# Kernel optimization log

Hardware: AMD Instinct MI355X
Metric: run time of the kernel (lower is better)

The kernel has to match this reference:

```python
import jax, jax.numpy as jnp
import numpy as np

V, D, HID, HOPS = 50000, 300, 300, 2
H = HID // 2  # per-direction hidden (bi_direction=True)
B, NT, SL, HL = 32, 20, 50, 50


def _gen_data():
    rng = np.random.default_rng(0)
    tc = np.zeros((B, NT, 3 + SL), np.int32)
    for b in range(B):
        tn = int(rng.integers(5, NT + 1))
        for t in range(tn):
            tc[b, t, :3] = rng.integers(1, 10, 3)
            sl = int(rng.integers(5, SL + 1))
            tc[b, t, 3:3 + sl] = rng.integers(1, V, sl)
    uh = np.zeros((B, HL, SL), np.int32)
    for b in range(B):
        hn = int(rng.integers(10, HL + 1))
        for s in range(hn):
            sl = int(rng.integers(5, SL + 1))
            uh[b, s, :sl] = rng.integers(1, V, sl)
    return jnp.asarray(tc), jnp.asarray(uh)


def setup_inputs():
    key = jax.random.key(0)
    ks = jax.random.split(key, 12)
    tc, uh = _gen_data()
    E = jax.random.normal(ks[0], (V, D), jnp.float32) * 0.05
    E = E.at[0].set(0.0)  # padding_idx=0
    nA = HOPS + 1  # hop_num+1 SentLSTM encoders (A[0] is also B)
    return {
        "target_conv": tc, "user_history": uh, "E": E,
        "A_Wih": jax.random.normal(ks[1], (nA, 2, 4 * H, D), jnp.float32) * 0.05,
        "A_Whh": jax.random.normal(ks[2], (nA, 2, 4 * H, H), jnp.float32) * 0.05,
        "A_bih": jax.random.normal(ks[3], (nA, 2, 4 * H), jnp.float32) * 0.05,
        "A_bhh": jax.random.normal(ks[4], (nA, 2, 4 * H), jnp.float32) * 0.05,
        "C_Wih": jax.random.normal(ks[5], (2, 4 * H, HID + 3), jnp.float32) * 0.05,
        "C_Whh": jax.random.normal(ks[6], (2, 4 * H, H), jnp.float32) * 0.05,
        "C_bih": jax.random.normal(ks[7], (2, 4 * H), jnp.float32) * 0.05,
        "C_bhh": jax.random.normal(ks[8], (2, 4 * H), jnp.float32) * 0.05,
        "W_out": jax.random.normal(ks[9], (HID,), jnp.float32) * 0.05,
        "b_out": jnp.zeros((), jnp.float32),
    }


def _lstm_final(x, lens, Wih, Whh, bih, bhh):
    """Masked-length LSTM over padded batch. x:[N,T,Din] -> final h:[N,H].
    PyTorch gate order i,f,g,o. Zero initial state. Updates frozen at t>=len."""
    N, T, _ = x.shape
    gx = jnp.einsum('ntd,gd->ntg', x, Wih) + bih  # input projection once

    def step(carry, inp):
        h, c = carry
        g_t, t = inp
        g = g_t + h @ Whh.T + bhh
        i, f, gg, o = jnp.split(g, 4, axis=-1)
        c_new = jax.nn.sigmoid(f) * c + jax.nn.sigmoid(i) * jnp.tanh(gg)
        h_new = jax.nn.sigmoid(o) * jnp.tanh(c_new)
        m = (t < lens)[:, None]
        return (jnp.where(m, h_new, h), jnp.where(m, c_new, c)), None

    h0 = jnp.zeros((N, Whh.shape[1]), x.dtype)
    (h, _), _ = jax.lax.scan(step, (h0, h0), (gx.transpose(1, 0, 2), jnp.arange(T)))
    return h


def _bilstm_final(x, lens, Wih, Whh, bih, bhh):
    """Bidirectional final hidden = concat(h_fwd_last_valid, h_bwd_after_full_reverse).
    Equivalent to pack_padded_sequence + nn.LSTM(bidirectional=True) final hidden."""
    T = x.shape[1]
    hf = _lstm_final(x, lens, Wih[0], Whh[0], bih[0], bhh[0])
    idx = jnp.clip(lens[:, None] - 1 - jnp.arange(T)[None, :], 0, T - 1)  # per-sample reverse
    hb = _lstm_final(jnp.take_along_axis(x, idx[:, :, None], axis=1), lens,
                     Wih[1], Whh[1], bih[1], bhh[1])
    return jnp.concatenate([hf, hb], axis=-1)


def reference(target_conv, user_history, E, A_Wih, A_Whh, A_bih, A_bhh,
              C_Wih, C_Whh, C_bih, C_bhh, W_out, b_out):
    # --- encode target conversation turns with B = A[0] ---
    tok = target_conv[:, :, 3:]                      # [B,NT,SL]
    slens = jnp.sum(tok != 0, -1).reshape(-1)        # ragged sentence lengths
    x = E[tok.reshape(B * NT, SL)]                   # [B*NT,SL,D]
    sent_reps = _bilstm_final(x, slens, A_Wih[0], A_Whh[0], A_bih[0], A_bhh[0]).reshape(B, NT, HID)
    feats = jnp.concatenate([sent_reps, target_conv[:, :, :3].astype(jnp.float32)], -1)  # [B,NT,HID+3]
    clens = jnp.sum(target_conv[:, :, 3] != 0, -1)   # valid turns per conv
    u = _bilstm_final(feats, clens, C_Wih, C_Whh, C_bih, C_bhh)  # [B,HID]
    # --- memory hops over user history ---
    hlens = jnp.sum(user_history != 0, -1).reshape(-1)
    hx = E[user_history.reshape(B * HL, SL)]
    reps = [_bilstm_final(hx, hlens, A_Wih[k], A_Whh[k], A_bih[k], A_bhh[k]).reshape(B, HL, HID)
            for k in range(HOPS + 1)]                # invalid sents have len=0 -> zero reps (matches zero-padding)
    for hop in range(HOPS):
        prob = jax.nn.softmax(jnp.einsum('bnd,bd->bn', reps[hop], u), -1)
        u = jnp.einsum('bn,bnd->bd', prob, reps[hop + 1]) + u
    return jax.nn.sigmoid(u @ W_out + b_out)
```

## Files before the change

### kernel.cpp

```cpp
#include <hip/hip_runtime.h>
#include <hip/hip_cooperative_groups.h>

typedef short v8s __attribute__((ext_vector_type(8)));
typedef float v4f __attribute__((ext_vector_type(4)));
typedef unsigned short ushort_t;
typedef unsigned int uint_t;

namespace cg = cooperative_groups;

__device__ inline ushort_t f2bf(float f) {
    union { float f; uint_t u; } v; v.f = f;
    uint_t r = v.u + 0x7FFFu + ((v.u >> 16) & 1u);
    return (ushort_t)(r >> 16);
}
__device__ inline float bf2f(ushort_t h) {
    union { uint_t u; float f; } v; v.u = ((uint_t)h) << 16;
    return v.f;
}
__device__ inline float sigf(float x) { return 1.f / (1.f + __expf(-x)); }
__device__ inline float tanh_f(float x) {
    float e = __expf(-2.f * x);
    return (1.f - e) / (1.f + e);
}

__global__ void k_lens(const int* __restrict__ tc, const int* __restrict__ uh,
                       int* lens_s, int* lens_h, int* lens_c) {
    int t = blockIdx.x * 256 + threadIdx.x;
    if (t < 640) {
        int c = 0;
        for (int s = 0; s < 50; ++s) c += (tc[t * 53 + 3 + s] != 0);
        lens_s[t] = c;
    } else if (t < 2240) {
        int r = t - 640; int c = 0;
        for (int s = 0; s < 50; ++s) c += (uh[r * 50 + s] != 0);
        lens_h[r] = c;
    } else if (t < 2272) {
        int b = t - 2240; int c = 0;
        for (int tt = 0; tt < 20; ++tt) c += (tc[(b * 20 + tt) * 53 + 3] != 0);
        lens_c[b] = c;
    }
}

__global__ void k_sort(const int* __restrict__ lens, int n,
                       int* __restrict__ perm, int* __restrict__ slen) {
    int i = blockIdx.x * 256 + threadIdx.x;
    if (i >= n) return;
    int li = lens[i]; int r = 0;
    for (int j = 0; j < n; ++j) {
        int lj = lens[j];
        r += (lj > li) || (lj == li && j < i);
    }
    perm[r] = i; slen[r] = li;
}

__global__ void k_packA(const float* __restrict__ Wih, const float* __restrict__ Whh,
                        const float* __restrict__ bih, const float* __restrict__ bhh,
                        ushort_t* __restrict__ pack) {
    int job = blockIdx.x; int lane = threadIdx.x;
    int set = job / 570; int rem = job % 570; int tile = rem / 15; int kc = rem % 15;
    int np = tile * 16 + (lane & 15);
    int g = np & 3, d = np >> 2;
    int orig = g * 150 + d;
    int kbase = kc * 32 + (lane >> 4) * 8;
    ushort_t v[8];
#pragma unroll
    for (int j = 0; j < 8; ++j) {
        int k = kbase + j; float f = 0.f;
        if (np < 600) {
            if (k < 300) f = Wih[((size_t)set * 600 + orig) * 300 + k];
            else if (k == 300) f = bih[set * 600 + orig] + bhh[set * 600 + orig];
            else if (k >= 320 && k < 470) f = Whh[((size_t)set * 600 + orig) * 150 + (k - 320)];
        }
        v[j] = f2bf(f);
    }
    uint4 u;
    u.x = (uint_t)v[0] | ((uint_t)v[1] << 16);
    u.y = (uint_t)v[2] | ((uint_t)v[3] << 16);
    u.z = (uint_t)v[4] | ((uint_t)v[5] << 16);
    u.w = (uint_t)v[6] | ((uint_t)v[7] << 16);
    *(uint4*)(pack + ((size_t)job * 64 + lane) * 8) = u;
}

__global__ void k_packC(const float* __restrict__ Wih, const float* __restrict__ Whh,
                        const float* __restrict__ bih, const float* __restrict__ bhh,
                        ushort_t* __restrict__ pack) {
    int job = blockIdx.x; int lane = threadIdx.x;
    int dir = job / 570; int rem = job % 570; int tile = rem / 15; int kc = rem % 15;
    int np = tile * 16 + (lane & 15);
    int g = np & 3, d = np >> 2;
    int orig = g * 150 + d;
    int kbase = kc * 32 + (lane >> 4) * 8;
    ushort_t v[8];
#pragma unroll
    for (int j = 0; j < 8; ++j) {
        int k = kbase + j; float f = 0.f;
        if (np < 600) {
            if (k < 303) f = Wih[((size_t)dir * 600 + orig) * 303 + k];
            else if (k == 303) f = bih[dir * 600 + orig] + bhh[dir * 600 + orig];
            else if (k >= 320 && k < 470) f = Whh[((size_t)dir * 600 + orig) * 150 + (k - 320)];
        }
        v[j] = f2bf(f);
    }
    uint4 u;
    u.x = (uint_t)v[0] | ((uint_t)v[1] << 16);
    u.y = (uint_t)v[2] | ((uint_t)v[3] << 16);
    u.z = (uint_t)v[4] | ((uint_t)v[5] << 16);
    u.w = (uint_t)v[6] | ((uint_t)v[7] << 16);
    *(uint4*)(pack + ((size_t)job * 64 + lane) * 8) = u;
}

__launch_bounds__(512, 2)
__global__ void k_main(const int* __restrict__ tcg, const int* __restrict__ uhg,
                       const float* __restrict__ E,
                       const int* __restrict__ perm_s, const int* __restrict__ slen_s,
                       const int* __restrict__ perm_h, const int* __restrict__ hlen_s,
                       const ushort_t* __restrict__ packA,
                       ushort_t* __restrict__ gx,
                       float* __restrict__ srep, float* __restrict__ reps,
                       int TC, int nchunks) {
    const int bid = blockIdx.x;
    const int tid = threadIdx.x;
    const int lane = tid & 63, w = tid >> 6, q = lane >> 4, l16 = lane & 15;

    __shared__ ushort_t H[64][168];
    __shared__ __align__(16) float Gp[8][16][68];

    const int isrec = (bid < 170);
    int r_pos0 = 0, r_windex = 0, r_dir = 0;
    const int* r_lenv = slen_s; const int* r_permv = perm_s;
    float* r_outp = srep;
    if (isrec) {
        if (bid < 20) {
            int grp = bid / 10; r_dir = grp; r_windex = grp; r_pos0 = (bid % 10) * 64;
            r_lenv = slen_s; r_permv = perm_s; r_outp = srep;
        } else {
            int gh = (bid - 20) / 25; r_windex = gh; r_dir = gh & 1;
            r_pos0 = ((bid - 20) % 25) * 64;
            r_lenv = hlen_s; r_permv = perm_h;
            r_outp = reps + (size_t)(gh >> 1) * 1600 * 300;
        }
        for (int i = tid; i < 64 * 84; i += 512) ((uint_t*)H)[i] = 0u;
    }
    int len4[4];
    if (isrec) {
#pragma unroll
        for (int i = 0; i < 4; ++i) len4[i] = r_lenv[r_pos0 + l16 + 16 * i];
    }
    float cst[5][4];
#pragma unroll
    for (int j = 0; j < 5; ++j)
#pragma unroll
        for (int i = 0; i < 4; ++i) cst[j][i] = 0.f;

    cg::grid_group grid = cg::this_grid();

    for (int c = 0; c < nchunks; ++c) {
        const int tcs0 = 50 - c * TC;
        const int tcs = tcs0 < TC ? tcs0 : TC;
        {
            const int nstepblk = (tcs + 3) / 4;
            const int njobs = 170 * nstepblk;
            for (int job = bid; job < njobs; job += 256) {
                int gj = job % 170; int sb = job / 170;
                const int* lenv; const int* permv; int pos0, windex, dir, isS;
                if (gj < 20) {
                    int grp = gj / 10; dir = grp; windex = grp; pos0 = (gj % 10) * 64;
                    lenv = slen_s; permv = perm_s; isS = 1;
                } else {
                    int gh = (gj - 20) / 25; windex = gh; dir = gh & 1;
                    pos0 = ((gj - 20) % 25) * 64;
                    lenv = hlen_s; permv = perm_h; isS = 0;
                }
                if (lenv[pos0] <= c * TC) continue;
                int lt = sb * 4 + (w >> 1);
                if (lt >= tcs) continue;
                int t = c * TC + lt;
                const int mh = (w & 1) * 2;

                v8s a[2][10];
#pragma unroll
                for (int mg = 0; mg < 2; ++mg) {
                    int pos = pos0 + (mh + mg) * 16 + l16;
                    int len = lenv[pos];
                    int tau = dir ? (len - 1 - t) : t;
                    tau = tau < 0 ? 0 : (tau > 49 ? 49 : tau);
                    int orig = permv[pos];
                    int tok = isS ? tcg[orig * 53 + 3 + tau] : uhg[orig * 50 + tau];
                    const float* Er = E + (size_t)tok * 300;
#pragma unroll
                    for (int kc = 0; kc < 9; ++kc) {
                        int k0 = kc * 32 + q * 8;
                        float4 f0 = *(const float4*)(Er + k0);
                        float4 f1 = *(const float4*)(Er + k0 + 4);
                        v8s r;
                        r[0] = (short)f2bf(f0.x); r[1] = (short)f2bf(f0.y);
                        r[2] = (short)f2bf(f0.z); r[3] = (short)f2bf(f0.w);
                        r[4] = (short)f2bf(f1.x); r[5] = (short)f2bf(f1.y);
                        r[6] = (short)f2bf(f1.z); r[7] = (short)f2bf(f1.w);
                        a[mg][kc] = r;
                    }
                    {
                        v8s r = (v8s){0,0,0,0,0,0,0,0};
                        if (q == 0) {
                            float4 f0 = *(const float4*)(Er + 288);
                            float4 f1 = *(const float4*)(Er + 292);
                            r[0] = (short)f2bf(f0.x); r[1] = (short)f2bf(f0.y);
                            r[2] = (short)f2bf(f0.z); r[3] = (short)f2bf(f0.w);
                            r[4] = (short)f2bf(f1.x); r[5] = (short)f2bf(f1.y);
                            r[6] = (short)f2bf(f1.z); r[7] = (short)f2bf(f1.w);
                        } else if (q == 1) {
                            float4 f0 = *(const float4*)(Er + 296);
                            r[0] = (short)f2bf(f0.x); r[1] = (short)f2bf(f0.y);
                            r[2] = (short)f2bf(f0.z); r[3] = (short)f2bf(f0.w);
                            r[4] = (short)0x3F80;
                        }
                        a[mg][9] = r;
                    }
                }

                const ushort_t* W = packA + (size_t)windex * 570 * 512;
                ushort_t* gout = gx + ((size_t)gj * TC + lt) * 38 * 1024;

                v8s bA[10], bB[10];
                auto loadB = [&](v8s* dst, int tn) {
                    const ushort_t* p = W + (size_t)tn * 15 * 512 + lane * 8;
#pragma unroll
                    for (int kc = 0; kc < 10; ++kc) dst[kc] = *(const v8s*)(p + (size_t)kc * 512);
                };
                auto compute = [&](int tn, v8s* b) {
                    v4f acc[2];
#pragma unroll
                    for (int mg = 0; mg < 2; ++mg) acc[mg] = (v4f){0.f, 0.f, 0.f, 0.f};
#pragma unroll
                    for (int kc = 0; kc < 10; ++kc)
#pragma unroll
                        for (int mg = 0; mg < 2; ++mg)
                            acc[mg] = __builtin_amdgcn_mfma_f32_16x16x32_bf16(a[mg][kc], b[kc], acc[mg], 0, 0, 0);
                    ushort_t* gt = gout + tn * 1024 + l16;
#pragma unroll
                    for (int mg = 0; mg < 2; ++mg)
#pragma unroll
                        for (int r = 0; r < 4; ++r)
                            gt[((mh + mg) * 16 + q * 4 + r) * 16] = f2bf(acc[mg][r]);
                };
                loadB(bA, 0);
                for (int tn = 0; tn < 38; tn += 2) {
                    loadB(bB, tn + 1 < 38 ? tn + 1 : 37);
                    compute(tn, bA);
                    loadB(bA, tn + 2 < 38 ? tn + 2 : 37);
                    compute(tn + 1, bB);
                }
            }
        }
        grid.sync();
        if (isrec) {
            int blockmax = r_lenv[r_pos0];
            int steps = blockmax - c * TC;
            steps = steps < 0 ? 0 : (steps > tcs ? tcs : steps);
            if (steps > 0) {
                const ushort_t* wslot = packA + (size_t)r_windex * 570 * 512;
                const ushort_t* gslot = gx + (size_t)bid * TC * 38 * 1024;
                auto loadW = [&](int j, v8s (&dst)[5]) {
                    int tn = w + 8 * j; int tnc = tn > 37 ? 37 : tn;
                    const ushort_t* wp = wslot + (size_t)tnc * 15 * 512 + lane * 8;
#pragma unroll
                    for (int kc = 0; kc < 5; ++kc) dst[kc] = *(const v8s*)(wp + (size_t)(10 + kc) * 512);
                };
                for (int lt = 0; lt < steps; ++lt) {
                    int t = c * TC + lt;
                    const ushort_t* gstep = gslot + (size_t)lt * 38 * 1024;
                    auto loadG = [&](int j, ushort4 (&dst)[4]) {
                        int tn = w + 8 * j; int tnc = tn > 37 ? 37 : tn;
                        const ushort_t* gb = gstep + (size_t)tnc * 1024 + q * 4;
#pragma unroll
                        for (int i = 0; i < 4; ++i)
                            dst[i] = *(const ushort4*)(gb + (l16 + 16 * i) * 16);
                    };
                    v8s wbA[5], wbB[5];
                    ushort4 gqA[4], gqB[4];
                    loadW(0, wbA); loadG(0, gqA);
                    __syncthreads();
                    v8s ah[4][5];
#pragma unroll
                    for (int mtg = 0; mtg < 4; ++mtg)
#pragma unroll
                        for (int kc = 0; kc < 5; ++kc)
                            ah[mtg][kc] = *(const v8s*)&H[mtg * 16 + l16][kc * 32 + q * 8];
                    __syncthreads();
                    auto jbody = [&](int j, v8s (&wcur)[5], ushort4 (&gcur)[4],
                                     v8s (&wnxt)[5], ushort4 (&gnxt)[4]) {
                        if (j < 4) { loadW(j + 1, wnxt); loadG(j + 1, gnxt); }
                        int tn = w + 8 * j;
                        if (tn < 38) {
                            v4f acc[4];
#pragma unroll
                            for (int mtg = 0; mtg < 4; ++mtg) acc[mtg] = (v4f){0.f, 0.f, 0.f, 0.f};
#pragma unroll
                            for (int kc = 0; kc < 5; ++kc)
#pragma unroll
                                for (int mtg = 0; mtg < 4; ++mtg)
                                    acc[mtg] = __builtin_amdgcn_mfma_f32_16x16x32_bf16(ah[mtg][kc], wcur[kc], acc[mtg], 0, 0, 0);
#pragma unroll
                            for (int mtg = 0; mtg < 4; ++mtg)
                                *(v4f*)&Gp[w][l16][mtg * 16 + q * 4] = acc[mtg];
                            int d = 4 * tn + q;
#pragma unroll
                            for (int i = 0; i < 4; ++i) {
                                int m = l16 + 16 * i;
                                if (t < len4[i]) {
                                    float gi = bf2f(gcur[i].x) + Gp[w][q * 4 + 0][m];
                                    float gf = bf2f(gcur[i].y) + Gp[w][q * 4 + 1][m];
                                    float gg = bf2f(gcur[i].z) + Gp[w][q * 4 + 2][m];
                                    float go = bf2f(gcur[i].w) + Gp[w][q * 4 + 3][m];
                                    float cn = sigf(gf) * cst[j][i] + sigf(gi) * tanh_f(gg);
                                    cst[j][i] = cn;
                                    if (d < 150) H[m][d] = f2bf(sigf(go) * tanh_f(cn));
                                }
                            }
                        }
                    };
                    jbody(0, wbA, gqA, wbB, gqB);
                    jbody(1, wbB, gqB, wbA, gqA);
                    jbody(2, wbA, gqA, wbB, gqB);
                    jbody(3, wbB, gqB, wbA, gqA);
                    jbody(4, wbA, gqA, wbB, gqB);
                }
                __syncthreads();
            }
        }
        grid.sync();
    }
    if (isrec) {
        int m = tid >> 3, dc = tid & 7;
        int orig = r_permv[r_pos0 + m];
#pragma unroll
        for (int k = 0; k < 19; ++k) {
            int d = dc + 8 * k;
            if (d < 150) r_outp[(size_t)orig * 300 + r_dir * 150 + d] = bf2f(H[m][d]);
        }
    }
}

__launch_bounds__(256, 1)
__global__ void k_gxc(const float* __restrict__ srep, const int* __restrict__ tcg,
                      const int* __restrict__ lens_c, const ushort_t* __restrict__ packC,
                      ushort_t* __restrict__ gxc) {
    const int dir = blockIdx.y;
    const int R0 = blockIdx.x * 256;
    const int tnbase = blockIdx.z * 2;
    const int tid = threadIdx.x, lane = tid & 63, w = tid >> 6, q = lane >> 4, l16 = lane & 15;

    v8s a[4][10];
#pragma unroll
    for (int mtg = 0; mtg < 4; ++mtg) {
        int R = R0 + w * 64 + mtg * 16 + l16;
        R = R < 639 ? R : 639;
        int b = R / 20, t = R % 20;
        int clen = lens_c[b];
        int te = dir ? (clen - 1 - t) : t;
        te = te < 0 ? 0 : (te > 19 ? 19 : te);
        const float* sr = srep + (size_t)(b * 20 + te) * 300;
        const int* ft = tcg + (size_t)(b * 20 + te) * 53;
#pragma unroll
        for (int kc = 0; kc < 9; ++kc) {
            int k0 = kc * 32 + q * 8;
            float4 f0 = *(const float4*)(sr + k0);
            float4 f1 = *(const float4*)(sr + k0 + 4);
            v8s r;
            r[0] = (short)f2bf(f0.x); r[1] = (short)f2bf(f0.y);
            r[2] = (short)f2bf(f0.z); r[3] = (short)f2bf(f0.w);
            r[4] = (short)f2bf(f1.x); r[5] = (short)f2bf(f1.y);
            r[6] = (short)f2bf(f1.z); r[7] = (short)f2bf(f1.w);
            a[mtg][kc] = r;
        }
        {
            v8s r = (v8s){0,0,0,0,0,0,0,0};
            if (q == 0) {
                float4 f0 = *(const float4*)(sr + 288);
                float4 f1 = *(const float4*)(sr + 292);
                r[0] = (short)f2bf(f0.x); r[1] = (short)f2bf(f0.y);
                r[2] = (short)f2bf(f0.z); r[3] = (short)f2bf(f0.w);
                r[4] = (short)f2bf(f1.x); r[5] = (short)f2bf(f1.y);
                r[6] = (short)f2bf(f1.z); r[7] = (short)f2bf(f1.w);
            } else if (q == 1) {
                float4 f0 = *(const float4*)(sr + 296);
                r[0] = (short)f2bf(f0.x); r[1] = (short)f2bf(f0.y);
                r[2] = (short)f2bf(f0.z); r[3] = (short)f2bf(f0.w);
                r[4] = (short)f2bf((float)ft[0]);
                r[5] = (short)f2bf((float)ft[1]);
                r[6] = (short)f2bf((float)ft[2]);
                r[7] = (short)0x3F80;
            }
            a[mtg][9] = r;
        }
    }
    const ushort_t* W = packC + (size_t)dir * 570 * 512;
    v8s bA[10];
    auto loadB = [&](v8s* dst, int tn) {
        const ushort_t* p = W + (size_t)tn * 15 * 512 + lane * 8;
#pragma unroll
        for (int kc = 0; kc < 10; ++kc) dst[kc] = *(const v8s*)(p + (size_t)kc * 512);
    };
    auto compute = [&](int tn, v8s* b) {
        v4f acc[4];
#pragma unroll
        for (int mtg = 0; mtg < 4; ++mtg) acc[mtg] = (v4f){0.f, 0.f, 0.f, 0.f};
#pragma unroll
        for (int kc = 0; kc < 10; ++kc)
#pragma unroll
            for (int mtg = 0; mtg < 4; ++mtg)
                acc[mtg] = __builtin_amdgcn_mfma_f32_16x16x32_bf16(a[mtg][kc], b[kc], acc[mtg], 0, 0, 0);
#pragma unroll
        for (int mtg = 0; mtg < 4; ++mtg)
#pragma unroll
            for (int r = 0; r < 4; ++r) {
                int R = R0 + w * 64 + mtg * 16 + q * 4 + r;
                if (R < 640) {
                    int b = R / 20, t = R % 20;
                    gxc[(((size_t)(dir * 20 + t) * 38 + tn) << 9) + b * 16 + l16] = f2bf(acc[mtg][r]);
                }
            }
    };
    for (int tn = tnbase; tn < tnbase + 2; ++tn) {
        loadB(bA, tn);
        compute(tn, bA);
    }
}

__launch_bounds__(256, 1)
__global__ void k_rec_c(const ushort_t* __restrict__ gxc, const int* __restrict__ lens_c,
                        const ushort_t* __restrict__ packC, float* __restrict__ out) {
    const int dir = blockIdx.x;
    const int tid = threadIdx.x, lane = tid & 63, w = tid >> 6, q = lane >> 4, l16 = lane & 15;

    __shared__ ushort_t H[32][168];
    __shared__ __align__(16) float Gp[4][16][68];
    __shared__ int lensl[32];
    __shared__ int mxs;

    if (tid < 32) lensl[tid] = lens_c[tid];
    for (int i = tid; i < 32 * 84; i += 256) ((uint_t*)H)[i] = 0u;
    __syncthreads();
    if (tid == 0) {
        int mx = 0;
        for (int i = 0; i < 32; ++i) mx = max(mx, lensl[i]);
        mxs = mx;
    }
    __syncthreads();
    const int maxlen = mxs;
    int len2[2];
#pragma unroll
    for (int i = 0; i < 2; ++i) len2[i] = lensl[i * 16 + l16];

    v8s wb[10][5];
#pragma unroll
    for (int j = 0; j < 10; ++j) {
        int tn = w + 4 * j; int tnc = tn > 37 ? 37 : tn;
        const ushort_t* wp = packC + (size_t)dir * 570 * 512 + (size_t)tnc * 15 * 512 + lane * 8;
#pragma unroll
        for (int kc = 0; kc < 5; ++kc) wb[j][kc] = *(const v8s*)(wp + (size_t)(10 + kc) * 512);
    }
    float cst[10][2];
#pragma unroll
    for (int j = 0; j < 10; ++j)
#pragma unroll
        for (int i = 0; i < 2; ++i) cst[j][i] = 0.f;

    for (int t = 0; t < maxlen; ++t) {
        __syncthreads();
        v8s ah[2][5];
#pragma unroll
        for (int mtg = 0; mtg < 2; ++mtg)
#pragma unroll
            for (int kc = 0; kc < 5; ++kc)
                ah[mtg][kc] = *(const v8s*)&H[mtg * 16 + l16][kc * 32 + q * 8];
        __syncthreads();
#pragma unroll
        for (int j = 0; j < 10; ++j) {
            int tn = w + 4 * j;
            if (tn < 38) {
                v4f acc[2];
#pragma unroll
                for (int mtg = 0; mtg < 2; ++mtg) acc[mtg] = (v4f){0.f, 0.f, 0.f, 0.f};
#pragma unroll
                for (int kc = 0; kc < 5; ++kc)
#pragma unroll
                    for (int mtg = 0; mtg < 2; ++mtg)
                        acc[mtg] = __builtin_amdgcn_mfma_f32_16x16x32_bf16(ah[mtg][kc], wb[j][kc], acc[mtg], 0, 0, 0);
#pragma unroll
                for (int mtg = 0; mtg < 2; ++mtg)
                    *(v4f*)&Gp[w][l16][mtg * 16 + q * 4] = acc[mtg];
                int d = 4 * tn + q;
                const ushort_t* gbase = gxc + (((size_t)(dir * 20 + t) * 38 + tn) << 9) + q * 4;
#pragma unroll
                for (int i = 0; i < 2; ++i) {
                    int m = l16 + 16 * i;
                    if (t < len2[i]) {
                        ushort4 gv = *(const ushort4*)(gbase + m * 16);
                        float gi = bf2f(gv.x) + Gp[w][q * 4 + 0][m];
                        float gf = bf2f(gv.y) + Gp[w][q * 4 + 1][m];
                        float gg = bf2f(gv.z) + Gp[w][q * 4 + 2][m];
                        float go = bf2f(gv.w) + Gp[w][q * 4 + 3][m];
                        float cn = sigf(gf) * cst[j][i] + sigf(gi) * tanh_f(gg);
                        cst[j][i] = cn;
                        if (d < 150) H[m][d] = f2bf(sigf(go) * tanh_f(cn));
                    }
                }
            }
        }
    }
    __syncthreads();
    {
        int m = tid >> 3;
#pragma unroll
        for (int k = 0; k < 19; ++k) {
            int d = (tid & 7) + 8 * k;
            if (d < 150) out[(size_t)m * 300 + dir * 150 + d] = bf2f(H[m][d]);
        }
    }
}

__global__ void k_attn(const float* __restrict__ reps, const float* __restrict__ u_in,
                       const float* __restrict__ Wout, const float* __restrict__ bout,
                       float* __restrict__ out) {
    const int b = blockIdx.x;
    const int tid = threadIdx.x;
    const int wave = tid >> 6, lane = tid & 63;
    __shared__ float u_l[300];
    __shared__ float dots[64];
    __shared__ float red[4];
    for (int d = tid; d < 300; d += 256) u_l[d] = u_in[b * 300 + d];
    __syncthreads();
    for (int hop = 0; hop < 2; ++hop) {
        const float* R0 = reps + ((size_t)hop * 1600 + b * 50) * 300;
        for (int n = wave; n < 50; n += 4) {
            float p = 0.f;
            for (int d = lane; d < 300; d += 64) p += R0[(size_t)n * 300 + d] * u_l[d];
            for (int off = 32; off > 0; off >>= 1) p += __shfl_down(p, off);
            if (lane == 0) dots[n] = p;
        }
        __syncthreads();
        if (tid < 64) {
            float x = (lane < 50) ? dots[lane] : -3.4e38f;
            float mx = x;
            for (int off = 32; off > 0; off >>= 1) mx = fmaxf(mx, __shfl_down(mx, off));
            mx = __shfl(mx, 0);
            float e = (lane < 50) ? __expf(x - mx) : 0.f;
            float s = e;
            for (int off = 32; off > 0; off >>= 1) s += __shfl_down(s, off);
            s = __shfl(s, 0);
            if (lane < 50) dots[lane] = e / s;
        }
        __syncthreads();
        const float* R1 = reps + ((size_t)(hop + 1) * 1600 + b * 50) * 300;
        for (int d = tid; d < 300; d += 256) {
            float s = 0.f;
            for (int n = 0; n < 50; ++n) s += dots[n] * R1[(size_t)n * 300 + d];
            u_l[d] += s;
        }
        __syncthreads();
    }
    float acc = 0.f;
    for (int d = tid; d < 300; d += 256) acc += u_l[d] * Wout[d];
    for (int off = 32; off > 0; off >>= 1) acc += __shfl_down(acc, off);
    if (lane == 0) red[wave] = acc;
    __syncthreads();
    if (tid == 0) {
        float s = red[0] + red[1] + red[2] + red[3] + bout[0];
        out[b] = 1.f / (1.f + __expf(-s));
    }
}

extern "C" void kernel_launch(void* const* d_in, const int* in_sizes, int n_in,
                              void* d_out, int out_size, void* d_ws, size_t ws_size,
                              hipStream_t stream) {
    (void)in_sizes; (void)n_in; (void)out_size;
    const int*   tc   = (const int*)d_in[0];
    const int*   uh   = (const int*)d_in[1];
    const float* E    = (const float*)d_in[2];
    const float* AWih = (const float*)d_in[3];
    const float* AWhh = (const float*)d_in[4];
    const float* Abih = (const float*)d_in[5];
    const float* Abhh = (const float*)d_in[6];
    const float* CWih = (const float*)d_in[7];
    const float* CWhh = (const float*)d_in[8];
    const float* Cbih = (const float*)d_in[9];
    const float* Cbhh = (const float*)d_in[10];
    const float* Wout = (const float*)d_in[11];
    const float* bout = (const float*)d_in[12];
    float* out = (float*)d_out;

    char* ws = (char*)d_ws;
    size_t off = 0;
    auto take = [&](size_t bytes) -> char* {
        char* p = ws + off;
        off = (off + bytes + 255) & ~(size_t)255;
        return p;
    };
    int* lens_s = (int*)take(640 * 4);
    int* lens_h = (int*)take(1600 * 4);
    int* lens_c = (int*)take(32 * 4);
    int* perm_s = (int*)take(640 * 4);
    int* slen_sorted = (int*)take(640 * 4);
    int* perm_h = (int*)take(1600 * 4);
    int* hlen_sorted = (int*)take(1600 * 4);
    ushort_t* packA = (ushort_t*)take((size_t)6 * 570 * 512 * 2);
    ushort_t* packC = (ushort_t*)take((size_t)2 * 570 * 512 * 2);
    float* srep = (float*)take((size_t)640 * 300 * 4);
    float* reps = (float*)take((size_t)3 * 1600 * 300 * 4);
    float* ubuf = (float*)take((size_t)32 * 300 * 4);
    ushort_t* gxc = (ushort_t*)take((size_t)2 * 20 * 38 * 1024);

    int TC = 1;
    for (int cand = 50; cand >= 1; --cand) {
        size_t need = off + (size_t)170 * cand * 38 * 2048 + 1024;
        if (need <= ws_size) { TC = cand; break; }
    }
    if (TC > 8) TC = 8;
    ushort_t* gx = (ushort_t*)take((size_t)170 * TC * 38 * 2048);
    int nchunks = (50 + TC - 1) / TC;

    k_lens<<<9, 256, 0, stream>>>(tc, uh, lens_s, lens_h, lens_c);
    k_sort<<<3, 256, 0, stream>>>(lens_s, 640, perm_s, slen_sorted);
    k_sort<<<7, 256, 0, stream>>>(lens_h, 1600, perm_h, hlen_sorted);
    k_packA<<<3420, 64, 0, stream>>>(AWih, AWhh, Abih, Abhh, packA);
    k_packC<<<1140, 64, 0, stream>>>(CWih, CWhh, Cbih, Cbhh, packC);

    {
        void* args[] = { (void*)&tc, (void*)&uh, (void*)&E,
                         (void*)&perm_s, (void*)&slen_sorted,
                         (void*)&perm_h, (void*)&hlen_sorted,
                         (void*)&packA, (void*)&gx, (void*)&srep, (void*)&reps,
                         (void*)&TC, (void*)&nchunks };
        hipLaunchCooperativeKernel((const void*)k_main, dim3(256), dim3(512),
                                   args, 0, stream);
    }

    k_gxc<<<dim3(3, 2, 19), 256, 0, stream>>>(srep, tc, lens_c, packC, gxc);
    k_rec_c<<<2, 256, 0, stream>>>(gxc, lens_c, packC, ubuf);
    k_attn<<<32, 256, 0, stream>>>(reps, ubuf, Wout, bout, out);
}
```

Baseline: 2.055 ms.

## Fuse input projection into per-step recurrence, drop cooperative grid sync and gx buffer

Replaces the chunked cooperative kernel, which precomputed input-gate projections into a global gx buffer and then ran the recurrence with grid.sync between phases, with a plain launch of 170 blocks of 256 threads. Each block now gathers embeddings and computes the input projection plus the hidden projection together every timestep with MFMA, keeping the cell state in registers. This removes grid-wide barriers and the global round trip of gate activations. In exchange the input projection now sits on the sequential critical path, each wave handles 19 gate tiles with 15-chunk weight loads per step, and register pressure is higher.

```diff
diff --git a/kernel.cpp b/kernel.cpp
--- a/kernel.cpp
+++ b/kernel.cpp
@@ -1,12 +1,9 @@
 #include <hip/hip_runtime.h>
-#include <hip/hip_cooperative_groups.h>
 
 typedef short v8s __attribute__((ext_vector_type(8)));
 typedef float v4f __attribute__((ext_vector_type(4)));
 typedef unsigned short ushort_t;
 typedef unsigned int uint_t;
-
-namespace cg = cooperative_groups;
 
 __device__ inline ushort_t f2bf(float f) {
     union { float f; uint_t u; } v; v.f = f;
@@ -109,233 +106,160 @@
     *(uint4*)(pack + ((size_t)job * 64 + lane) * 8) = u;
 }
 
-__launch_bounds__(512, 2)
+__launch_bounds__(256, 1)
 __global__ void k_main(const int* __restrict__ tcg, const int* __restrict__ uhg,
                        const float* __restrict__ E,
                        const int* __restrict__ perm_s, const int* __restrict__ slen_s,
                        const int* __restrict__ perm_h, const int* __restrict__ hlen_s,
                        const ushort_t* __restrict__ packA,
-                       ushort_t* __restrict__ gx,
-                       float* __restrict__ srep, float* __restrict__ reps,
-                       int TC, int nchunks) {
+                       float* __restrict__ srep, float* __restrict__ reps) {
     const int bid = blockIdx.x;
     const int tid = threadIdx.x;
     const int lane = tid & 63, w = tid >> 6, q = lane >> 4, l16 = lane & 15;
+    const int u = w >> 1;
+    const int h19 = (w & 1) * 19;
 
     __shared__ ushort_t H[64][168];
-    __shared__ __align__(16) float Gp[8][16][68];
-
-    const int isrec = (bid < 170);
-    int r_pos0 = 0, r_windex = 0, r_dir = 0;
-    const int* r_lenv = slen_s; const int* r_permv = perm_s;
-    float* r_outp = srep;
-    if (isrec) {
-        if (bid < 20) {
-            int grp = bid / 10; r_dir = grp; r_windex = grp; r_pos0 = (bid % 10) * 64;
-            r_lenv = slen_s; r_permv = perm_s; r_outp = srep;
-        } else {
-            int gh = (bid - 20) / 25; r_windex = gh; r_dir = gh & 1;
-            r_pos0 = ((bid - 20) % 25) * 64;
-            r_lenv = hlen_s; r_permv = perm_h;
-            r_outp = reps + (size_t)(gh >> 1) * 1600 * 300;
-        }
-        for (int i = tid; i < 64 * 84; i += 512) ((uint_t*)H)[i] = 0u;
-    }
-    int len4[4];
-    if (isrec) {
-#pragma unroll
-        for (int i = 0; i < 4; ++i) len4[i] = r_lenv[r_pos0 + l16 + 16 * i];
-    }
-    float cst[5][4];
-#pragma unroll
-    for (int j = 0; j < 5; ++j)
-#pragma unroll
-        for (int i = 0; i < 4; ++i) cst[j][i] = 0.f;
-
-    cg::grid_group grid = cg::this_grid();
-
-    for (int c = 0; c < nchunks; ++c) {
-        const int tcs0 = 50 - c * TC;
-        const int tcs = tcs0 < TC ? tcs0 : TC;
-        {
-            const int nstepblk = (tcs + 3) / 4;
-            const int njobs = 170 * nstepblk;
-            for (int job = bid; job < njobs; job += 256) {
-                int gj = job % 170; int sb = job / 170;
-                const int* lenv; const int* permv; int pos0, windex, dir, isS;
-                if (gj < 20) {
-                    int grp = gj / 10; dir = grp; windex = grp; pos0 = (gj % 10) * 64;
-                    lenv = slen_s; permv = perm_s; isS = 1;
-                } else {
-                    int gh = (gj - 20) / 25; windex = gh; dir = gh & 1;
-                    pos0 = ((gj - 20) % 25) * 64;
-                    lenv = hlen_s; permv = perm_h; isS = 0;
+    __shared__ __align__(16) float Gp[4][16][68];
+
+    int r_pos0, r_windex, r_dir, isS;
+    const int* r_lenv; const int* r_permv;
+    float* r_outp;
+    if (bid < 20) {
+        int grp = bid / 10; r_dir = grp; r_windex = grp; r_pos0 = (bid % 10) * 64;
+        r_lenv = slen_s; r_permv = perm_s; r_outp = srep; isS = 1;
+    } else {
+        int gh = (bid - 20) / 25; r_windex = gh; r_dir = gh & 1;
+        r_pos0 = ((bid - 20) % 25) * 64;
+        r_lenv = hlen_s; r_permv = perm_h;
+        r_outp = reps + (size_t)(gh >> 1) * 1600 * 300; isS = 0;
+    }
+    for (int i = tid; i < 64 * 84; i += 256) ((uint_t*)H)[i] = 0u;
+
+    int lenm[2]; const int* tokp[2];
+#pragma unroll
+    for (int mg = 0; mg < 2; ++mg) {
+        int pos = r_pos0 + u * 32 + mg * 16 + l16;
+        lenm[mg] = r_lenv[pos];
+        int orig = r_permv[pos];
+        tokp[mg] = isS ? (tcg + (size_t)orig * 53 + 3) : (uhg + (size_t)orig * 50);
+    }
+    float cst[19][2];
+#pragma unroll
+    for (int j = 0; j < 19; ++j)
+#pragma unroll
+        for (int i = 0; i < 2; ++i) cst[j][i] = 0.f;
+
+    const int blockmax = r_lenv[r_pos0];
+    const ushort_t* wslot = packA + (size_t)r_windex * 570 * 512;
+
+    auto loadW = [&](int j, v8s (&dst)[15]) {
+        int tn = h19 + j;
+        const ushort_t* wp = wslot + (size_t)tn * 15 * 512 + lane * 8;
+#pragma unroll
+        for (int kc = 0; kc < 15; ++kc) dst[kc] = *(const v8s*)(wp + (size_t)kc * 512);
+    };
+
+    __syncthreads();
+
+    for (int t = 0; t < blockmax; ++t) {
+        v8s a[2][10];
+#pragma unroll
+        for (int mg = 0; mg < 2; ++mg) {
+            int tau = r_dir ? (lenm[mg] - 1 - t) : t;
+            tau = tau < 0 ? 0 : (tau > 49 ? 49 : tau);
+            int tok = tokp[mg][tau];
+            const float* Er = E + (size_t)tok * 300;
+#pragma unroll
+            for (int kc = 0; kc < 9; ++kc) {
+                int k0 = kc * 32 + q * 8;
+                float4 f0 = *(const float4*)(Er + k0);
+                float4 f1 = *(const float4*)(Er + k0 + 4);
+                v8s r;
+                r[0] = (short)f2bf(f0.x); r[1] = (short)f2bf(f0.y);
+                r[2] = (short)f2bf(f0.z); r[3] = (short)f2bf(f0.w);
+                r[4] = (short)f2bf(f1.x); r[5] = (short)f2bf(f1.y);
+                r[6] = (short)f2bf(f1.z); r[7] = (short)f2bf(f1.w);
+                a[mg][kc] = r;
+            }
+            {
+                v8s r = (v8s){0,0,0,0,0,0,0,0};
+                if (q == 0) {
+                    float4 f0 = *(const float4*)(Er + 288);
+                    float4 f1 = *(const float4*)(Er + 292);
+                    r[0] = (short)f2bf(f0.x); r[1] = (short)f2bf(f0.y);
+                    r[2] = (short)f2bf(f0.z); r[3] = (short)f2bf(f0.w);
+                    r[4] = (short)f2bf(f1.x); r[5] = (short)f2bf(f1.y);
+                    r[6] = (short)f2bf(f1.z); r[7] = (short)f2bf(f1.w);
+                } else if (q == 1) {
+                    float4 f0 = *(const float4*)(Er + 296);
+                    r[0] = (short)f2bf(f0.x); r[1] = (short)f2bf(f0.y);
+                    r[2] = (short)f2bf(f0.z); r[3] = (short)f2bf(f0.w);
+                    r[4] = (short)0x3F80;
                 }
-                if (lenv[pos0] <= c * TC) continue;
-                int lt = sb * 4 + (w >> 1);
-                if (lt >= tcs) continue;
-                int t = c * TC + lt;
-                const int mh = (w & 1) * 2;
-
-                v8s a[2][10];
-#pragma unroll
-                for (int mg = 0; mg < 2; ++mg) {
-                    int pos = pos0 + (mh + mg) * 16 + l16;
-                    int len = lenv[pos];
-                    int tau = dir ? (len - 1 - t) : t;
-                    tau = tau < 0 ? 0 : (tau > 49 ? 49 : tau);
-                    int orig = permv[pos];
-                    int tok = isS ? tcg[orig * 53 + 3 + tau] : uhg[orig * 50 + tau];
-                    const float* Er = E + (size_t)tok * 300;
-#pragma unroll
-                    for (int kc = 0; kc < 9; ++kc) {
-                        int k0 = kc * 32 + q * 8;
-                        float4 f0 = *(const float4*)(Er + k0);
-                        float4 f1 = *(const float4*)(Er + k0 + 4);
-                        v8s r;
-                        r[0] = (short)f2bf(f0.x); r[1] = (short)f2bf(f0.y);
-                        r[2] = (short)f2bf(f0.z); r[3] = (short)f2bf(f0.w);
-                        r[4] = (short)f2bf(f1.x); r[5] = (short)f2bf(f1.y);
-                        r[6] = (short)f2bf(f1.z); r[7] = (short)f2bf(f1.w);
-                        a[mg][kc] = r;
-                    }
-                    {
-                        v8s r = (v8s){0,0,0,0,0,0,0,0};
-                        if (q == 0) {
-                            float4 f0 = *(const float4*)(Er + 288);
-                            float4 f1 = *(const float4*)(Er + 292);
-                            r[0] = (short)f2bf(f0.x); r[1] = (short)f2bf(f0.y);
-                            r[2] = (short)f2bf(f0.z); r[3] = (short)f2bf(f0.w);
-                            r[4] = (short)f2bf(f1.x); r[5] = (short)f2bf(f1.y);
-                            r[6] = (short)f2bf(f1.z); r[7] = (short)f2bf(f1.w);
-                        } else if (q == 1) {
-                            float4 f0 = *(const float4*)(Er + 296);
-                            r[0] = (short)f2bf(f0.x); r[1] = (short)f2bf(f0.y);
-                            r[2] = (short)f2bf(f0.z); r[3] = (short)f2bf(f0.w);
-                            r[4] = (short)0x3F80;
-                        }
-                        a[mg][9] = r;
-                    }
-                }
-
-                const ushort_t* W = packA + (size_t)windex * 570 * 512;
-                ushort_t* gout = gx + ((size_t)gj * TC + lt) * 38 * 1024;
-
-                v8s bA[10], bB[10];
-                auto loadB = [&](v8s* dst, int tn) {
-                    const ushort_t* p = W + (size_t)tn * 15 * 512 + lane * 8;
-#pragma unroll
-                    for (int kc = 0; kc < 10; ++kc) dst[kc] = *(const v8s*)(p + (size_t)kc * 512);
-                };
-                auto compute = [&](int tn, v8s* b) {
-                    v4f acc[2];
-#pragma unroll
-                    for (int mg = 0; mg < 2; ++mg) acc[mg] = (v4f){0.f, 0.f, 0.f, 0.f};
-#pragma unroll
-                    for (int kc = 0; kc < 10; ++kc)
-#pragma unroll
-                        for (int mg = 0; mg < 2; ++mg)
-                            acc[mg] = __builtin_amdgcn_mfma_f32_16x16x32_bf16(a[mg][kc], b[kc], acc[mg], 0, 0, 0);
-                    ushort_t* gt = gout + tn * 1024 + l16;
-#pragma unroll
-                    for (int mg = 0; mg < 2; ++mg)
-#pragma unroll
-                        for (int r = 0; r < 4; ++r)
-                            gt[((mh + mg) * 16 + q * 4 + r) * 16] = f2bf(acc[mg][r]);
-                };
-                loadB(bA, 0);
-                for (int tn = 0; tn < 38; tn += 2) {
-                    loadB(bB, tn + 1 < 38 ? tn + 1 : 37);
-                    compute(tn, bA);
-                    loadB(bA, tn + 2 < 38 ? tn + 2 : 37);
-                    compute(tn + 1, bB);
+                a[mg][9] = r;
+            }
+        }
+
+        v8s wA[15], wB[15];
+        loadW(0, wA);
+        __syncthreads();
+        v8s ah[2][5];
+#pragma unroll
+        for (int mg = 0; mg < 2; ++mg)
+#pragma unroll
+            for (int kc = 0; kc < 5; ++kc)
+                ah[mg][kc] = *(const v8s*)&H[u * 32 + mg * 16 + l16][kc * 32 + q * 8];
+        __syncthreads();
+
+        auto jbody = [&](int j, v8s (&wcur)[15], v8s (&wnxt)[15]) {
+            if (j < 18) loadW(j + 1, wnxt);
+            int tn = h19 + j;
+            v4f acc[2];
+#pragma unroll
+            for (int mg = 0; mg < 2; ++mg) acc[mg] = (v4f){0.f, 0.f, 0.f, 0.f};
+#pragma unroll
+            for (int kc = 0; kc < 10; ++kc)
+#pragma unroll
+                for (int mg = 0; mg < 2; ++mg)
+                    acc[mg] = __builtin_amdgcn_mfma_f32_16x16x32_bf16(a[mg][kc], wcur[kc], acc[mg], 0, 0, 0);
+#pragma unroll
+            for (int kc = 0; kc < 5; ++kc)
+#pragma unroll
+                for (int mg = 0; mg < 2; ++mg)
+                    acc[mg] = __builtin_amdgcn_mfma_f32_16x16x32_bf16(ah[mg][kc], wcur[10 + kc], acc[mg], 0, 0, 0);
+#pragma unroll
+            for (int mg = 0; mg < 2; ++mg)
+                *(v4f*)&Gp[w][l16][mg * 16 + q * 4] = acc[mg];
+            int d = 4 * tn + q;
+#pragma unroll
+            for (int i = 0; i < 2; ++i) {
+                int mloc = l16 + 16 * i;
+                if (t < lenm[i]) {
+                    float gi = Gp[w][q * 4 + 0][mloc];
+                    float gf = Gp[w][q * 4 + 1][mloc];
+                    float gg = Gp[w][q * 4 + 2][mloc];
+                    float go = Gp[w][q * 4 + 3][mloc];
+                    float cn = sigf(gf) * cst[j][i] + sigf(gi) * tanh_f(gg);
+                    cst[j][i] = cn;
+                    if (d < 150) H[u * 32 + mloc][d] = f2bf(sigf(go) * tanh_f(cn));
                 }
             }
-        }
-        grid.sync();
-        if (isrec) {
-            int blockmax = r_lenv[r_pos0];
-            int steps = blockmax - c * TC;
-            steps = steps < 0 ? 0 : (steps > tcs ? tcs : steps);
-            if (steps > 0) {
-                const ushort_t* wslot = packA + (size_t)r_windex * 570 * 512;
-                const ushort_t* gslot = gx + (size_t)bid * TC * 38 * 1024;
-                auto loadW = [&](int j, v8s (&dst)[5]) {
-                    int tn = w + 8 * j; int tnc = tn > 37 ? 37 : tn;
-                    const ushort_t* wp = wslot + (size_t)tnc * 15 * 512 + lane * 8;
-#pragma unroll
-                    for (int kc = 0; kc < 5; ++kc) dst[kc] = *(const v8s*)(wp + (size_t)(10 + kc) * 512);
-                };
-                for (int lt = 0; lt < steps; ++lt) {
-                    int t = c * TC + lt;
-                    const ushort_t* gstep = gslot + (size_t)lt * 38 * 1024;
-                    auto loadG = [&](int j, ushort4 (&dst)[4]) {
-                        int tn = w + 8 * j; int tnc = tn > 37 ? 37 : tn;
-                        const ushort_t* gb = gstep + (size_t)tnc * 1024 + q * 4;
-#pragma unroll
-                        for (int i = 0; i < 4; ++i)
-                            dst[i] = *(const ushort4*)(gb + (l16 + 16 * i) * 16);
-                    };
-                    v8s wbA[5], wbB[5];
-                    ushort4 gqA[4], gqB[4];
-                    loadW(0, wbA); loadG(0, gqA);
-                    __syncthreads();
-                    v8s ah[4][5];
-#pragma unroll
-                    for (int mtg = 0; mtg < 4; ++mtg)
-#pragma unroll
-                        for (int kc = 0; kc < 5; ++kc)
-                            ah[mtg][kc] = *(const v8s*)&H[mtg * 16 + l16][kc * 32 + q * 8];
-                    __syncthreads();
-                    auto jbody = [&](int j, v8s (&wcur)[5], ushort4 (&gcur)[4],
-                                     v8s (&wnxt)[5], ushort4 (&gnxt)[4]) {
-                        if (j < 4) { loadW(j + 1, wnxt); loadG(j + 1, gnxt); }
-                        int tn = w + 8 * j;
-                        if (tn < 38) {
-                            v4f acc[4];
-#pragma unroll
-                            for (int mtg = 0; mtg < 4; ++mtg) acc[mtg] = (v4f){0.f, 0.f, 0.f, 0.f};
-#pragma unroll
-                            for (int kc = 0; kc < 5; ++kc)
-#pragma unroll
-                                for (int mtg = 0; mtg < 4; ++mtg)
-                                    acc[mtg] = __builtin_amdgcn_mfma_f32_16x16x32_bf16(ah[mtg][kc], wcur[kc], acc[mtg], 0, 0, 0);
-#pragma unroll
-                            for (int mtg = 0; mtg < 4; ++mtg)
-                                *(v4f*)&Gp[w][l16][mtg * 16 + q * 4] = acc[mtg];
-                            int d = 4 * tn + q;
-#pragma unroll
-                            for (int i = 0; i < 4; ++i) {
-                                int m = l16 + 16 * i;
-                                if (t < len4[i]) {
-                                    float gi = bf2f(gcur[i].x) + Gp[w][q * 4 + 0][m];
-                                    float gf = bf2f(gcur[i].y) + Gp[w][q * 4 + 1][m];
-                                    float gg = bf2f(gcur[i].z) + Gp[w][q * 4 + 2][m];
-                                    float go = bf2f(gcur[i].w) + Gp[w][q * 4 + 3][m];
-                                    float cn = sigf(gf) * cst[j][i] + sigf(gi) * tanh_f(gg);
-                                    cst[j][i] = cn;
-                                    if (d < 150) H[m][d] = f2bf(sigf(go) * tanh_f(cn));
-                                }
-                            }
-                        }
-                    };
-                    jbody(0, wbA, gqA, wbB, gqB);
-                    jbody(1, wbB, gqB, wbA, gqA);
-                    jbody(2, wbA, gqA, wbB, gqB);
-                    jbody(3, wbB, gqB, wbA, gqA);
-                    jbody(4, wbA, gqA, wbB, gqB);
-                }
-                __syncthreads();
-            }
-        }
-        grid.sync();
-    }
-    if (isrec) {
-        int m = tid >> 3, dc = tid & 7;
+        };
+        jbody(0, wA, wB);  jbody(1, wB, wA);  jbody(2, wA, wB);  jbody(3, wB, wA);
+        jbody(4, wA, wB);  jbody(5, wB, wA);  jbody(6, wA, wB);  jbody(7, wB, wA);
+        jbody(8, wA, wB);  jbody(9, wB, wA);  jbody(10, wA, wB); jbody(11, wB, wA);
+        jbody(12, wA, wB); jbody(13, wB, wA); jbody(14, wA, wB); jbody(15, wB, wA);
+        jbody(16, wA, wB); jbody(17, wB, wA); jbody(18, wA, wB);
+    }
+    __syncthreads();
+
+    {
+        int m = tid >> 2, dc = tid & 3;
         int orig = r_permv[r_pos0 + m];
 #pragma unroll
-        for (int k = 0; k < 19; ++k) {
-            int d = dc + 8 * k;
+        for (int k = 0; k < 38; ++k) {
+            int d = dc + 4 * k;
             if (d < 150) r_outp[(size_t)orig * 300 + r_dir * 150 + d] = bf2f(H[m][d]);
         }
     }
@@ -574,7 +498,7 @@
 extern "C" void kernel_launch(void* const* d_in, const int* in_sizes, int n_in,
                               void* d_out, int out_size, void* d_ws, size_t ws_size,
                               hipStream_t stream) {
-    (void)in_sizes; (void)n_in; (void)out_size;
+    (void)in_sizes; (void)n_in; (void)out_size; (void)ws_size;
     const int*   tc   = (const int*)d_in[0];
     const int*   uh   = (const int*)d_in[1];
     const float* E    = (const float*)d_in[2];
@@ -611,30 +535,15 @@
     float* ubuf = (float*)take((size_t)32 * 300 * 4);
     ushort_t* gxc = (ushort_t*)take((size_t)2 * 20 * 38 * 1024);
 
-    int TC = 1;
-    for (int cand = 50; cand >= 1; --cand) {
-        size_t need = off + (size_t)170 * cand * 38 * 2048 + 1024;
-        if (need <= ws_size) { TC = cand; break; }
-    }
-    if (TC > 8) TC = 8;
-    ushort_t* gx = (ushort_t*)take((size_t)170 * TC * 38 * 2048);
-    int nchunks = (50 + TC - 1) / TC;
-
     k_lens<<<9, 256, 0, stream>>>(tc, uh, lens_s, lens_h, lens_c);
     k_sort<<<3, 256, 0, stream>>>(lens_s, 640, perm_s, slen_sorted);
     k_sort<<<7, 256, 0, stream>>>(lens_h, 1600, perm_h, hlen_sorted);
     k_packA<<<3420, 64, 0, stream>>>(AWih, AWhh, Abih, Abhh, packA);
     k_packC<<<1140, 64, 0, stream>>>(CWih, CWhh, Cbih, Cbhh, packC);
 
-    {
-        void* args[] = { (void*)&tc, (void*)&uh, (void*)&E,
-                         (void*)&perm_s, (void*)&slen_sorted,
-                         (void*)&perm_h, (void*)&hlen_sorted,
-                         (void*)&packA, (void*)&gx, (void*)&srep, (void*)&reps,
-                         (void*)&TC, (void*)&nchunks };
-        hipLaunchCooperativeKernel((const void*)k_main, dim3(256), dim3(512),
-                                   args, 0, stream);
-    }
+    k_main<<<170, 256, 0, stream>>>(tc, uh, E,
+                                    perm_s, slen_sorted, perm_h, hlen_sorted,
+                                    packA, srep, reps);
 
     k_gxc<<<dim3(3, 2, 19), 256, 0, stream>>>(srep, tc, lens_c, packC, gxc);
     k_rec_c<<<2, 256, 0, stream>>>(gxc, lens_c, packC, ubuf);
```

Result: slower. 4.635 ms (+125.6%).
